# Kernel tuning notes

Measured on AMD Instinct MI355X. Metric: run time of the kernel, lower is better.

The kernel has to match this reference:

```python
import jax, jax.numpy as jnp
import numpy as np

B, NPTS, NBASIS, DIM, H, CH = 8, 1024, 8, 8, 512, 16
EPSILON = 1000.0
P = 2
VOLUME = 2.0 ** DIM  # MC domain [-1,1]^dim


def setup_inputs() -> dict:
    key = jax.random.key(0)
    ks = jax.random.split(key, 10)
    s = jax.random.uniform(ks[0], (NPTS, DIM), dtype=jnp.float32) * 2.0 - 1.0  # MC samples in [-1,1]^dim
    x = jax.random.uniform(ks[1], (1, DIM), dtype=jnp.float32) * 2.0 - 1.0     # eval point
    Wfirst = jax.random.normal(ks[2], (DIM, H), dtype=jnp.float32) / np.sqrt(DIM)
    bfirst = jax.random.normal(ks[3], (H,), dtype=jnp.float32) * 0.01
    Wb = jax.random.normal(ks[4], (NBASIS, H, H), dtype=jnp.float32) / np.sqrt(H)
    bb = jax.random.normal(ks[5], (NBASIS, H), dtype=jnp.float32) * 0.01
    Wlast = jax.random.normal(ks[6], (H, CH), dtype=jnp.float32) / np.sqrt(H)
    blast = jax.random.normal(ks[7], (CH,), dtype=jnp.float32) * 0.01
    Wf = jax.random.normal(ks[8], (DIM, CH), dtype=jnp.float32) / np.sqrt(DIM)
    bf = jax.random.normal(ks[9], (CH,), dtype=jnp.float32) * 0.01
    return dict(s=s, x=x, Wfirst=Wfirst, bfirst=bfirst, Wb=Wb, bb=bb,
                Wlast=Wlast, blast=blast, Wf=Wf, bf=bf)


def _basis_all(pts, Wfirst, bfirst, Wb, bb, Wlast, blast):
    # pts: [M, DIM] -> all n basis nets, batch-repeated: [NBASIS, B, M, CH]
    a0 = jax.nn.elu(jnp.einsum('md,dh->mh', pts, Wfirst) + bfirst)          # [M, H]
    a0 = jnp.broadcast_to(a0[None], (B,) + a0.shape)                         # [B, M, H] (repeat over batch)
    a1 = jax.nn.elu(jnp.einsum('bmh,ihk->ibmk', a0, Wb) + bb[:, None, None, :])  # [n, B, M, H]
    return jnp.einsum('ibmk,kc->ibmc', a1, Wlast) + blast                    # [n, B, M, CH]


def reference(s, x, Wfirst, bfirst, Wb, bb, Wlast, blast, Wf, bf):
    # func(s): linear map realizing the projected function  [NPTS, CH]
    f_s = jnp.einsum('nd,dc->nc', s, Wf) + bf
    basis_s = _basis_all(s, Wfirst, bfirst, Wb, bb, Wlast, blast)            # [n, B, NPTS, CH]
    diff = f_s[None, None] - basis_s                                          # broadcast over n, B
    # Monte Carlo integral of (func - basis_i)^p over [-1,1]^dim, per channel
    integral = VOLUME * jnp.mean(diff ** P, axis=-2)                          # [n, B, CH]
    norm_pc = integral ** (1.0 / P)                                           # Lp norm per channel
    norm_b = jnp.sum(jnp.abs(norm_pc) ** P, axis=-1, keepdims=True) ** (1.0 / P)  # [n, B, 1]
    mu = jnp.where(norm_b <= EPSILON, norm_b, 0.0)                            # [n, B, 1]
    basis_x = _basis_all(x, Wfirst, bfirst, Wb, bb, Wlast, blast)[:, :, 0, :]  # [n, B, CH]
    out = jnp.sum(mu * basis_x, axis=0)                                       # [B, CH]
    normalization = 1e-7 + jnp.sum(mu, axis=0)                                # [B, 1]
    return out / normalization
```

## Files before the change

kernel.cpp:

```cpp
#include <hip/hip_runtime.h>

typedef _Float16 half8 __attribute__((ext_vector_type(8)));
typedef float f32x4 __attribute__((ext_vector_type(4)));
typedef float f32x16 __attribute__((ext_vector_type(16)));
typedef unsigned int u32x4 __attribute__((ext_vector_type(4)));

#define NPTS 1024
#define NB 8
#define HDIM 512
#define CH 16
#define RT 1056

#define OFF_WBF 0u
#define OFF_A0F (4u*1024u*1024u)
#define A0SZ    (64u*RT*16u)
#define OFF_WLF (OFF_A0F + A0SZ)
#define OFF_FS  (OFF_WLF + 16384u)
#define OFF_IS  (OFF_FS + 65536u)
#define OFF_BX  (OFF_IS + 64u)
#define OFF_CT  (OFF_BX + 512u)

__device__ __forceinline__ float elu(float z) { return z > 0.f ? z : expm1f(z); }

__global__ __launch_bounds__(256) void kPrep(const float* __restrict__ s,
    const float* __restrict__ x, const float* __restrict__ Wfirst,
    const float* __restrict__ bfirst, const float* __restrict__ Wb,
    const float* __restrict__ Wlast, const float* __restrict__ Wf,
    const float* __restrict__ bf,
    _Float16* __restrict__ Wbf, _Float16* __restrict__ Wlf,
    _Float16* __restrict__ a0f, float* __restrict__ f_s,
    float* __restrict__ Isum, unsigned* __restrict__ cnt) {
  __shared__ __align__(16) float sm[8192];
  int b = blockIdx.x, t = threadIdx.x;
  if (b < 1024) {
    int i = b >> 7, koct = (b >> 1) & 63, n = (b & 1) * 256 + t;
    const float* src = Wb + ((size_t)i * 512 + koct * 8) * 512 + n;
    float v[8];
#pragma unroll
    for (int j = 0; j < 8; ++j) v[j] = src[j * 512];
    union { _Float16 h[8]; u32x4 u; } hu;
#pragma unroll
    for (int j = 0; j < 8; ++j) hu.h[j] = (_Float16)v[j];
    *(u32x4*)(Wbf + ((size_t)(i * 64 + koct) * 512 + n) * 8) = hu.u;
  } else if (b < 1288) {
    int rr = t >> 6, tl = t & 63;
    int m = (b - 1024) * 4 + rr;
    float* sv = &sm[rr * 8];
    if (tl < 8) sv[tl] = (m < 1024) ? s[m * 8 + tl] : (m == 1024 ? x[tl] : 0.f);
    __syncthreads();
    size_t o = ((size_t)tl * RT + m) * 8;
    if (m <= 1024) {
      float acc[8];
#pragma unroll
      for (int jj = 0; jj < 8; ++jj) acc[jj] = bfirst[8 * tl + jj];
#pragma unroll
      for (int d = 0; d < 8; ++d) {
        float sd = sv[d];
        f32x4 w0 = *(const f32x4*)&Wfirst[d * 512 + 8 * tl];
        f32x4 w1 = *(const f32x4*)&Wfirst[d * 512 + 8 * tl + 4];
#pragma unroll
        for (int e = 0; e < 4; ++e) { acc[e] += sd * w0[e]; acc[4 + e] += sd * w1[e]; }
      }
      union { _Float16 h[8]; u32x4 u; } hu;
#pragma unroll
      for (int jj = 0; jj < 8; ++jj) hu.h[jj] = (_Float16)elu(acc[jj]);
      *(u32x4*)(a0f + o) = hu.u;
      if (m < 1024 && tl < 16) {
        float a = bf[tl];
#pragma unroll
        for (int d = 0; d < 8; ++d) a += sv[d] * Wf[d * 16 + tl];
        f_s[m * 16 + tl] = a;
      }
    } else {
      u32x4 z;
#pragma unroll
      for (int e = 0; e < 4; ++e) z[e] = 0u;
      *(u32x4*)(a0f + o) = z;
    }
  } else {
    if (t < 8) Isum[t] = 0.f;
    if (t == 8) *cnt = 0u;
#pragma unroll
    for (int it = 0; it < 32; ++it) sm[t + 256 * it] = Wlast[t + 256 * it];
    __syncthreads();
#pragma unroll
    for (int p = 0; p < 4; ++p) {
      int oi = p * 256 + t;
      int ko = oi >> 4, ch = oi & 15;
      union { _Float16 h[8]; u32x4 u; } hu;
#pragma unroll
      for (int jj = 0; jj < 8; ++jj) hu.h[jj] = (_Float16)sm[(ko * 8 + jj) * 16 + ch];
      *(u32x4*)(Wlf + oi * 8) = hu.u;
    }
  }
}

__global__ __launch_bounds__(1024, 4) void kB(const _Float16* __restrict__ Wbf,
    const _Float16* __restrict__ a0f, const _Float16* __restrict__ Wlf,
    const float* __restrict__ bb, const float* __restrict__ blast,
    const float* __restrict__ f_s, float* __restrict__ Isum,
    float* __restrict__ basisx, unsigned* __restrict__ cnt,
    float* __restrict__ out) {
  __shared__ u32x4 SC[2048];
  __shared__ float S2[32][16];
  __shared__ float wsum[16];
  __shared__ unsigned oc;
  __shared__ float muL[8];
  int t = threadIdx.x, b = blockIdx.x;
  int i = b & 7, mt = b >> 3;
  int m0 = mt * 32;
  int w = t >> 6, lane = t & 63, ln = lane & 31, q = lane >> 5, q4 = lane >> 4;
  int nw = w * 32;

  const u32x4* a4 = (const u32x4*)a0f;
  const u32x4* b4 = (const u32x4*)Wbf;
  int ma = m0 + ln, nb = nw + ln, ib = i * 64;

  f32x16 acc;
#pragma unroll
  for (int rr = 0; rr < 16; ++rr) acc[rr] = 0.f;

  u32x4 pa[4][2], pb[4][2];
#pragma unroll
  for (int st = 0; st < 3; ++st) {
    int k0 = st * 4 + q, k1 = k0 + 2;
    pa[st][0] = a4[k0 * RT + ma];
    pa[st][1] = a4[k1 * RT + ma];
    pb[st][0] = b4[(size_t)(ib + k0) * 512 + nb];
    pb[st][1] = b4[(size_t)(ib + k1) * 512 + nb];
  }
#pragma unroll
  for (int ks = 0; ks < 16; ++ks) {
    int sl = ks & 3;
    acc = __builtin_amdgcn_mfma_f32_32x32x16_f16(
        __builtin_bit_cast(half8, pa[sl][0]), __builtin_bit_cast(half8, pb[sl][0]), acc, 0, 0, 0);
    acc = __builtin_amdgcn_mfma_f32_32x32x16_f16(
        __builtin_bit_cast(half8, pa[sl][1]), __builtin_bit_cast(half8, pb[sl][1]), acc, 0, 0, 0);
    if (ks < 13) {
      int sn = (ks + 3) & 3;
      int k0 = (ks + 3) * 4 + q, k1 = k0 + 2;
      pa[sn][0] = a4[k0 * RT + ma];
      pa[sn][1] = a4[k1 * RT + ma];
      pb[sn][0] = b4[(size_t)(ib + k0) * 512 + nb];
      pb[sn][1] = b4[(size_t)(ib + k1) * 512 + nb];
    }
  }

  if (t < 512) ((float*)S2)[t] = 0.f;
  __syncthreads();

  float bcol = bb[i * 512 + nw + ln];
  _Float16* scr = (_Float16*)&SC[w * 128];
#pragma unroll
  for (int rr = 0; rr < 16; ++rr) {
    int row = (rr & 3) + 8 * (rr >> 2) + 4 * q;
    float a1 = elu(acc[rr] + bcol);
    int oi = (row >> 4) * 64 + (ln >> 3) * 16 + (row & 15);
    scr[oi * 8 + (ln & 7)] = (_Float16)a1;
  }
  __syncthreads();

  const u32x4* s4 = &SC[w * 128];
  const u32x4* w4 = (const u32x4*)Wlf;
  int ch = lane & 15;
  half8 wv = __builtin_bit_cast(half8, w4[(size_t)((nw >> 3) + q4) * 16 + ch]);
#pragma unroll
  for (int mt2 = 0; mt2 < 2; ++mt2) {
    f32x4 D2;
#pragma unroll
    for (int rr = 0; rr < 4; ++rr) D2[rr] = 0.f;
    half8 pv = __builtin_bit_cast(half8, s4[mt2 * 64 + q4 * 16 + ch]);
    D2 = __builtin_amdgcn_mfma_f32_16x16x32_f16(pv, wv, D2, 0, 0, 0);
#pragma unroll
    for (int rr = 0; rr < 4; ++rr)
      atomicAdd(&S2[mt2 * 16 + q4 * 4 + rr][ch], D2[rr]);
  }
  __syncthreads();

  if (mt == 32) {
    if (t < 16) basisx[i * 16 + t] = S2[0][t] + blast[t];
  } else {
    float loc = 0.f;
    if (t < 512) {
      int ml = t >> 4, c2 = t & 15;
      float bs = S2[ml][c2] + blast[c2];
      float d = f_s[(size_t)(m0 + ml) * 16 + c2] - bs;
      loc = d * d;
    }
    loc += __shfl_xor(loc, 1, 64);
    loc += __shfl_xor(loc, 2, 64);
    loc += __shfl_xor(loc, 4, 64);
    loc += __shfl_xor(loc, 8, 64);
    loc += __shfl_xor(loc, 16, 64);
    loc += __shfl_xor(loc, 32, 64);
    if (lane == 0) wsum[w] = loc;
    __syncthreads();
    if (t == 0) {
      float S = 0.f;
#pragma unroll
      for (int ww = 0; ww < 16; ++ww) S += wsum[ww];
      atomicAdd(&Isum[i], S);
    }
  }

  if (t == 0) {
    __threadfence();
    oc = atomicAdd(cnt, 1u);
  }
  __syncthreads();
  if (oc == 263) {
    __threadfence();
    if (t < 8) {
      float S = atomicAdd(&Isum[t], 0.f);
      float nb = 0.5f * sqrtf(S);
      muL[t] = (nb <= 1000.0f) ? nb : 0.f;
    }
    __syncthreads();
    if (t < 128) {
      int c2 = t & 15;
      float num = 0.f, den = 1e-7f;
#pragma unroll
      for (int ii = 0; ii < NB; ++ii) {
        float bx = atomicAdd(&basisx[ii * 16 + c2], 0.f);
        num += muL[ii] * bx;
        den += muL[ii];
      }
      out[t] = num / den;
    }
  }
}

extern "C" void kernel_launch(void* const* d_in, const int* in_sizes, int n_in,
                              void* d_out, int out_size, void* d_ws, size_t ws_size,
                              hipStream_t stream) {
  const float* s      = (const float*)d_in[0];
  const float* x      = (const float*)d_in[1];
  const float* Wfirst = (const float*)d_in[2];
  const float* bfirst = (const float*)d_in[3];
  const float* Wb     = (const float*)d_in[4];
  const float* bb     = (const float*)d_in[5];
  const float* Wlast  = (const float*)d_in[6];
  const float* blast  = (const float*)d_in[7];
  const float* Wf     = (const float*)d_in[8];
  const float* bf     = (const float*)d_in[9];

  char* ws = (char*)d_ws;
  _Float16* Wbf = (_Float16*)(ws + OFF_WBF);
  _Float16* a0f = (_Float16*)(ws + OFF_A0F);
  _Float16* Wlf = (_Float16*)(ws + OFF_WLF);
  float* f_s    = (float*)(ws + OFF_FS);
  float* Isum   = (float*)(ws + OFF_IS);
  float* basisx = (float*)(ws + OFF_BX);
  unsigned* cnt = (unsigned*)(ws + OFF_CT);
  float* out    = (float*)d_out;

  kPrep<<<1289, 256, 0, stream>>>(s, x, Wfirst, bfirst, Wb, Wlast, Wf, bf,
                                  Wbf, Wlf, a0f, f_s, Isum, cnt);
  kB<<<264, 1024, 0, stream>>>(Wbf, a0f, Wlf, bb, blast, f_s, Isum, basisx, cnt, out);
}
```

Before: 126.6 us.

## Stage GEMM operands through LDS with direct global-to-LDS loads

```diff
diff --git a/kernel.cpp b/kernel.cpp
--- a/kernel.cpp
+++ b/kernel.cpp
@@ -19,6 +19,10 @@
 #define OFF_IS  (OFF_FS + 65536u)
 #define OFF_BX  (OFF_IS + 64u)
 #define OFF_CT  (OFF_BX + 512u)
+
+#define GL2LDS(g, l) __builtin_amdgcn_global_load_lds( \
+    (const __attribute__((address_space(1))) void*)(g), \
+    (__attribute__((address_space(3))) void*)(l), 16, 0, 0)
 
 __device__ __forceinline__ float elu(float z) { return z > 0.f ? z : expm1f(z); }
 
@@ -101,56 +105,60 @@
     const float* __restrict__ f_s, float* __restrict__ Isum,
     float* __restrict__ basisx, unsigned* __restrict__ cnt,
     float* __restrict__ out) {
-  __shared__ u32x4 SC[2048];
-  __shared__ float S2[32][16];
-  __shared__ float wsum[16];
-  __shared__ unsigned oc;
-  __shared__ float muL[8];
+  __shared__ __align__(16) char ALDS[32768];
+  __shared__ __align__(16) char BLDS[32768];
   int t = threadIdx.x, b = blockIdx.x;
   int i = b & 7, mt = b >> 3;
   int m0 = mt * 32;
   int w = t >> 6, lane = t & 63, ln = lane & 31, q = lane >> 5, q4 = lane >> 4;
-  int nw = w * 32;
+  int nw = w * 32, nb = nw + ln, ib = i * 64;
 
   const u32x4* a4 = (const u32x4*)a0f;
   const u32x4* b4 = (const u32x4*)Wbf;
-  int ma = m0 + ln, nb = nw + ln, ib = i * 64;
+  const u32x4* Ald = (const u32x4*)ALDS;
+  const u32x4* Bld = (const u32x4*)BLDS;
+
+#pragma unroll
+  for (int it = 0; it < 2; ++it) {
+    int o = t + 1024 * it;
+    GL2LDS(a4 + ((size_t)(o >> 5) * RT + m0 + (o & 31)), ALDS + o * 16);
+    GL2LDS(b4 + ((size_t)ib * 512 + o), BLDS + o * 16);
+  }
+  __syncthreads();
 
   f32x16 acc;
 #pragma unroll
   for (int rr = 0; rr < 16; ++rr) acc[rr] = 0.f;
 
-  u32x4 pa[4][2], pb[4][2];
-#pragma unroll
-  for (int st = 0; st < 3; ++st) {
-    int k0 = st * 4 + q, k1 = k0 + 2;
-    pa[st][0] = a4[k0 * RT + ma];
-    pa[st][1] = a4[k1 * RT + ma];
-    pb[st][0] = b4[(size_t)(ib + k0) * 512 + nb];
-    pb[st][1] = b4[(size_t)(ib + k1) * 512 + nb];
-  }
-#pragma unroll
-  for (int ks = 0; ks < 16; ++ks) {
-    int sl = ks & 3;
-    acc = __builtin_amdgcn_mfma_f32_32x32x16_f16(
-        __builtin_bit_cast(half8, pa[sl][0]), __builtin_bit_cast(half8, pb[sl][0]), acc, 0, 0, 0);
-    acc = __builtin_amdgcn_mfma_f32_32x32x16_f16(
-        __builtin_bit_cast(half8, pa[sl][1]), __builtin_bit_cast(half8, pb[sl][1]), acc, 0, 0, 0);
-    if (ks < 13) {
-      int sn = (ks + 3) & 3;
-      int k0 = (ks + 3) * 4 + q, k1 = k0 + 2;
-      pa[sn][0] = a4[k0 * RT + ma];
-      pa[sn][1] = a4[k1 * RT + ma];
-      pb[sn][0] = b4[(size_t)(ib + k0) * 512 + nb];
-      pb[sn][1] = b4[(size_t)(ib + k1) * 512 + nb];
-    }
-  }
-
+  for (int c = 0; c < 16; ++c) {
+#pragma unroll
+    for (int s = 0; s < 2; ++s) {
+      int kr = s * 2 + q;
+      half8 aH = __builtin_bit_cast(half8, Ald[(c * 4 + kr) * 32 + ln]);
+      half8 bH = __builtin_bit_cast(half8, Bld[kr * 512 + nb]);
+      acc = __builtin_amdgcn_mfma_f32_32x32x16_f16(aH, bH, acc, 0, 0, 0);
+    }
+    __syncthreads();
+    if (c < 15) {
+#pragma unroll
+      for (int it = 0; it < 2; ++it) {
+        int o = t + 1024 * it;
+        GL2LDS(b4 + ((size_t)(ib + (c + 1) * 4) * 512 + o), BLDS + o * 16);
+      }
+      __syncthreads();
+    }
+  }
+  __syncthreads();
+
+  float (*S2)[16]   = (float(*)[16])ALDS;
+  float* wsum       = (float*)(ALDS + 2048);
+  float* muL        = (float*)(ALDS + 2112);
+  unsigned* ocp     = (unsigned*)(ALDS + 2176);
   if (t < 512) ((float*)S2)[t] = 0.f;
   __syncthreads();
 
   float bcol = bb[i * 512 + nw + ln];
-  _Float16* scr = (_Float16*)&SC[w * 128];
+  _Float16* scr = (_Float16*)(BLDS + w * 2048);
 #pragma unroll
   for (int rr = 0; rr < 16; ++rr) {
     int row = (rr & 3) + 8 * (rr >> 2) + 4 * q;
@@ -160,7 +168,7 @@
   }
   __syncthreads();
 
-  const u32x4* s4 = &SC[w * 128];
+  const u32x4* s4 = (const u32x4*)(BLDS + w * 2048);
   const u32x4* w4 = (const u32x4*)Wlf;
   int ch = lane & 15;
   half8 wv = __builtin_bit_cast(half8, w4[(size_t)((nw >> 3) + q4) * 16 + ch]);
@@ -205,15 +213,15 @@
 
   if (t == 0) {
     __threadfence();
-    oc = atomicAdd(cnt, 1u);
-  }
-  __syncthreads();
-  if (oc == 263) {
+    *ocp = atomicAdd(cnt, 1u);
+  }
+  __syncthreads();
+  if (*ocp == 263) {
     __threadfence();
     if (t < 8) {
       float S = atomicAdd(&Isum[t], 0.f);
-      float nb = 0.5f * sqrtf(S);
-      muL[t] = (nb <= 1000.0f) ? nb : 0.f;
+      float nbv = 0.5f * sqrtf(S);
+      muL[t] = (nbv <= 1000.0f) ? nbv : 0.f;
     }
     __syncthreads();
     if (t < 128) {
```

Measured after the change: 128.4 us. No clear change (+1.4%).

## Fuse first-layer activation into GEMM kernel and split hidden dim across blocks

Applied to the files above, without the earlier changes.

```diff
diff --git a/kernel.cpp b/kernel.cpp
--- a/kernel.cpp
+++ b/kernel.cpp
@@ -9,27 +9,21 @@
 #define NB 8
 #define HDIM 512
 #define CH 16
-#define RT 1056
 
 #define OFF_WBF 0u
-#define OFF_A0F (4u*1024u*1024u)
-#define A0SZ    (64u*RT*16u)
-#define OFF_WLF (OFF_A0F + A0SZ)
-#define OFF_FS  (OFF_WLF + 16384u)
-#define OFF_IS  (OFF_FS + 65536u)
-#define OFF_BX  (OFF_IS + 64u)
-#define OFF_CT  (OFF_BX + 512u)
+#define OFF_WLF 4194304u
+#define OFF_PP  4210688u
+#define OFF_IS  4751360u
+#define OFF_BX  4751424u
+#define OFF_GC  4751936u
 
 __device__ __forceinline__ float elu(float z) { return z > 0.f ? z : expm1f(z); }
 
-__global__ __launch_bounds__(256) void kPrep(const float* __restrict__ s,
-    const float* __restrict__ x, const float* __restrict__ Wfirst,
-    const float* __restrict__ bfirst, const float* __restrict__ Wb,
-    const float* __restrict__ Wlast, const float* __restrict__ Wf,
-    const float* __restrict__ bf,
+__global__ __launch_bounds__(256) void kPrep(const float* __restrict__ Wb,
+    const float* __restrict__ Wlast,
     _Float16* __restrict__ Wbf, _Float16* __restrict__ Wlf,
-    _Float16* __restrict__ a0f, float* __restrict__ f_s,
-    float* __restrict__ Isum, unsigned* __restrict__ cnt) {
+    float* __restrict__ Pp, float* __restrict__ Isum,
+    float* __restrict__ basisx, unsigned* __restrict__ gc) {
   __shared__ __align__(16) float sm[8192];
   int b = blockIdx.x, t = threadIdx.x;
   if (b < 1024) {
@@ -42,44 +36,11 @@
 #pragma unroll
     for (int j = 0; j < 8; ++j) hu.h[j] = (_Float16)v[j];
     *(u32x4*)(Wbf + ((size_t)(i * 64 + koct) * 512 + n) * 8) = hu.u;
-  } else if (b < 1288) {
-    int rr = t >> 6, tl = t & 63;
-    int m = (b - 1024) * 4 + rr;
-    float* sv = &sm[rr * 8];
-    if (tl < 8) sv[tl] = (m < 1024) ? s[m * 8 + tl] : (m == 1024 ? x[tl] : 0.f);
-    __syncthreads();
-    size_t o = ((size_t)tl * RT + m) * 8;
-    if (m <= 1024) {
-      float acc[8];
-#pragma unroll
-      for (int jj = 0; jj < 8; ++jj) acc[jj] = bfirst[8 * tl + jj];
-#pragma unroll
-      for (int d = 0; d < 8; ++d) {
-        float sd = sv[d];
-        f32x4 w0 = *(const f32x4*)&Wfirst[d * 512 + 8 * tl];
-        f32x4 w1 = *(const f32x4*)&Wfirst[d * 512 + 8 * tl + 4];
-#pragma unroll
-        for (int e = 0; e < 4; ++e) { acc[e] += sd * w0[e]; acc[4 + e] += sd * w1[e]; }
-      }
-      union { _Float16 h[8]; u32x4 u; } hu;
-#pragma unroll
-      for (int jj = 0; jj < 8; ++jj) hu.h[jj] = (_Float16)elu(acc[jj]);
-      *(u32x4*)(a0f + o) = hu.u;
-      if (m < 1024 && tl < 16) {
-        float a = bf[tl];
-#pragma unroll
-        for (int d = 0; d < 8; ++d) a += sv[d] * Wf[d * 16 + tl];
-        f_s[m * 16 + tl] = a;
-      }
-    } else {
-      u32x4 z;
-#pragma unroll
-      for (int e = 0; e < 4; ++e) z[e] = 0u;
-      *(u32x4*)(a0f + o) = z;
-    }
-  } else {
+  } else if (b == 1024) {
     if (t < 8) Isum[t] = 0.f;
-    if (t == 8) *cnt = 0u;
+    if (t < 128) basisx[t] = 0.f;
+    gc[t] = 0u;
+    if (t < 9) gc[256 + t] = 0u;
 #pragma unroll
     for (int it = 0; it < 32; ++it) sm[t + 256 * it] = Wlast[t + 256 * it];
     __syncthreads();
@@ -92,65 +53,108 @@
       for (int jj = 0; jj < 8; ++jj) hu.h[jj] = (_Float16)sm[(ko * 8 + jj) * 16 + ch];
       *(u32x4*)(Wlf + oi * 8) = hu.u;
     }
+  } else {
+    int o4 = (b - 1025) * 256 + t;
+    if (o4 < 33792) {
+      f32x4 z; z[0] = 0.f; z[1] = 0.f; z[2] = 0.f; z[3] = 0.f;
+      *(f32x4*)&Pp[o4 * 4] = z;
+    }
   }
 }
 
-__global__ __launch_bounds__(1024, 4) void kB(const _Float16* __restrict__ Wbf,
-    const _Float16* __restrict__ a0f, const _Float16* __restrict__ Wlf,
-    const float* __restrict__ bb, const float* __restrict__ blast,
-    const float* __restrict__ f_s, float* __restrict__ Isum,
-    float* __restrict__ basisx, unsigned* __restrict__ cnt,
-    float* __restrict__ out) {
-  __shared__ u32x4 SC[2048];
-  __shared__ float S2[32][16];
-  __shared__ float wsum[16];
-  __shared__ unsigned oc;
-  __shared__ float muL[8];
+__global__ __launch_bounds__(256, 4) void kB(const _Float16* __restrict__ Wbf,
+    const _Float16* __restrict__ Wlf, const float* __restrict__ s,
+    const float* __restrict__ x, const float* __restrict__ Wfirst,
+    const float* __restrict__ bfirst, const float* __restrict__ Wf,
+    const float* __restrict__ bf, const float* __restrict__ bb,
+    const float* __restrict__ blast, float* __restrict__ Pp,
+    float* __restrict__ Isum, float* __restrict__ basisx,
+    unsigned* __restrict__ gc, float* __restrict__ out) {
+  __shared__ __align__(16) char LB[32768 + 2048 + 256];
+  float* S2f   = (float*)(LB + 32768);
+  float* wsum  = (float*)(LB + 34816);
+  float* muL   = (float*)(LB + 34880);
+  unsigned* ocp  = (unsigned*)(LB + 34944);
+  unsigned* ocgp = (unsigned*)(LB + 34948);
+  const u32x4* Ald = (const u32x4*)LB;
+
   int t = threadIdx.x, b = blockIdx.x;
-  int i = b & 7, mt = b >> 3;
+  int i = b & 7, r = b >> 3;
+  int nq = r & 3, mt = r >> 2;
   int m0 = mt * 32;
   int w = t >> 6, lane = t & 63, ln = lane & 31, q = lane >> 5, q4 = lane >> 4;
-  int nw = w * 32;
-
-  const u32x4* a4 = (const u32x4*)a0f;
+  int nw = nq * 128 + w * 32;
+  int nb = nw + ln, ib = i * 64;
   const u32x4* b4 = (const u32x4*)Wbf;
-  int ma = m0 + ln, nb = nw + ln, ib = i * 64;
-
-  f32x16 acc;
-#pragma unroll
-  for (int rr = 0; rr < 16; ++rr) acc[rr] = 0.f;
-
-  u32x4 pa[4][2], pb[4][2];
+
+  {
+    int m = m0 + (t >> 3), d = t & 7;
+    S2f[t] = (m < 1024) ? s[m * 8 + d] : (m == 1024 ? x[d] : 0.f);
+  }
+
+  u32x4 pb[4][2];
 #pragma unroll
   for (int st = 0; st < 3; ++st) {
     int k0 = st * 4 + q, k1 = k0 + 2;
-    pa[st][0] = a4[k0 * RT + ma];
-    pa[st][1] = a4[k1 * RT + ma];
     pb[st][0] = b4[(size_t)(ib + k0) * 512 + nb];
     pb[st][1] = b4[(size_t)(ib + k1) * 512 + nb];
   }
+  __syncthreads();
+
+  {
+    int ml = t & 31, hq = t >> 5;
+    int hb = hq * 64;
+    float sr[8];
+#pragma unroll
+    for (int d = 0; d < 8; ++d) sr[d] = S2f[ml * 8 + d];
+#pragma unroll
+    for (int oj = 0; oj < 8; ++oj) {
+      int h0 = hb + oj * 8;
+      float a[8];
+      f32x4 b0 = *(const f32x4*)&bfirst[h0];
+      f32x4 b1 = *(const f32x4*)&bfirst[h0 + 4];
+#pragma unroll
+      for (int e = 0; e < 4; ++e) { a[e] = b0[e]; a[4 + e] = b1[e]; }
+#pragma unroll
+      for (int d = 0; d < 8; ++d) {
+        float sd = sr[d];
+        f32x4 w0 = *(const f32x4*)&Wfirst[d * 512 + h0];
+        f32x4 w1 = *(const f32x4*)&Wfirst[d * 512 + h0 + 4];
+#pragma unroll
+        for (int e = 0; e < 4; ++e) { a[e] += sd * w0[e]; a[4 + e] += sd * w1[e]; }
+      }
+      union { _Float16 h[8]; u32x4 u; } hu;
+#pragma unroll
+      for (int e = 0; e < 8; ++e) hu.h[e] = (_Float16)elu(a[e]);
+      ((u32x4*)LB)[(hq * 8 + oj) * 32 + ml] = hu.u;
+    }
+  }
+  __syncthreads();
+
+  f32x16 acc;
+#pragma unroll
+  for (int rr = 0; rr < 16; ++rr) acc[rr] = 0.f;
 #pragma unroll
   for (int ks = 0; ks < 16; ++ks) {
     int sl = ks & 3;
-    acc = __builtin_amdgcn_mfma_f32_32x32x16_f16(
-        __builtin_bit_cast(half8, pa[sl][0]), __builtin_bit_cast(half8, pb[sl][0]), acc, 0, 0, 0);
-    acc = __builtin_amdgcn_mfma_f32_32x32x16_f16(
-        __builtin_bit_cast(half8, pa[sl][1]), __builtin_bit_cast(half8, pb[sl][1]), acc, 0, 0, 0);
+    int k0 = ks * 4 + q, k1 = k0 + 2;
+    half8 aH0 = __builtin_bit_cast(half8, Ald[k0 * 32 + ln]);
+    half8 aH1 = __builtin_bit_cast(half8, Ald[k1 * 32 + ln]);
+    acc = __builtin_amdgcn_mfma_f32_32x32x16_f16(aH0, __builtin_bit_cast(half8, pb[sl][0]), acc, 0, 0, 0);
+    acc = __builtin_amdgcn_mfma_f32_32x32x16_f16(aH1, __builtin_bit_cast(half8, pb[sl][1]), acc, 0, 0, 0);
     if (ks < 13) {
       int sn = (ks + 3) & 3;
-      int k0 = (ks + 3) * 4 + q, k1 = k0 + 2;
-      pa[sn][0] = a4[k0 * RT + ma];
-      pa[sn][1] = a4[k1 * RT + ma];
-      pb[sn][0] = b4[(size_t)(ib + k0) * 512 + nb];
-      pb[sn][1] = b4[(size_t)(ib + k1) * 512 + nb];
-    }
-  }
-
-  if (t < 512) ((float*)S2)[t] = 0.f;
-  __syncthreads();
-
+      int kn0 = (ks + 3) * 4 + q, kn1 = kn0 + 2;
+      pb[sn][0] = b4[(size_t)(ib + kn0) * 512 + nb];
+      pb[sn][1] = b4[(size_t)(ib + kn1) * 512 + nb];
+    }
+  }
+  __syncthreads();
+
+  S2f[t] = 0.f;
+  S2f[t + 256] = 0.f;
   float bcol = bb[i * 512 + nw + ln];
-  _Float16* scr = (_Float16*)&SC[w * 128];
+  _Float16* scr = (_Float16*)(LB + w * 2048);
 #pragma unroll
   for (int rr = 0; rr < 16; ++rr) {
     int row = (rr & 3) + 8 * (rr >> 2) + 4 * q;
@@ -160,10 +164,11 @@
   }
   __syncthreads();
 
-  const u32x4* s4 = &SC[w * 128];
+  const u32x4* s4 = (const u32x4*)(LB + w * 2048);
   const u32x4* w4 = (const u32x4*)Wlf;
   int ch = lane & 15;
   half8 wv = __builtin_bit_cast(half8, w4[(size_t)((nw >> 3) + q4) * 16 + ch]);
+  float (*S2)[16] = (float(*)[16])S2f;
 #pragma unroll
   for (int mt2 = 0; mt2 < 2; ++mt2) {
     f32x4 D2;
@@ -177,55 +182,63 @@
   }
   __syncthreads();
 
-  if (mt == 32) {
-    if (t < 16) basisx[i * 16 + t] = S2[0][t] + blast[t];
-  } else {
-    float loc = 0.f;
-    if (t < 512) {
-      int ml = t >> 4, c2 = t & 15;
-      float bs = S2[ml][c2] + blast[c2];
-      float d = f_s[(size_t)(m0 + ml) * 16 + c2] - bs;
-      loc = d * d;
-    }
-    loc += __shfl_xor(loc, 1, 64);
-    loc += __shfl_xor(loc, 2, 64);
-    loc += __shfl_xor(loc, 4, 64);
-    loc += __shfl_xor(loc, 8, 64);
-    loc += __shfl_xor(loc, 16, 64);
-    loc += __shfl_xor(loc, 32, 64);
-    if (lane == 0) wsum[w] = loc;
+  float* pp = Pp + (size_t)(i * 33 + mt) * 512;
+#pragma unroll
+  for (int p = 0; p < 2; ++p) atomicAdd(&pp[t + 256 * p], S2f[t + 256 * p]);
+  __threadfence();
+  if (t == 0) *ocp = atomicAdd(&gc[mt * 8 + i], 1u);
+  __syncthreads();
+
+  if (*ocp == 3) {
+    __threadfence();
+    if (mt == 32) {
+      if (t < 16) atomicAdd(&basisx[i * 16 + t], atomicAdd(&pp[t], 0.f) + blast[t]);
+    } else {
+      float loc = 0.f;
+#pragma unroll
+      for (int p = 0; p < 2; ++p) {
+        int o = t + 256 * p;
+        int ml = o >> 4, c2 = o & 15;
+        int gm = m0 + ml;
+        float fs = bf[c2];
+#pragma unroll
+        for (int d = 0; d < 8; ++d) fs += s[gm * 8 + d] * Wf[d * 16 + c2];
+        float bs = atomicAdd(&pp[o], 0.f) + blast[c2];
+        float dd = fs - bs;
+        loc += dd * dd;
+      }
+      loc += __shfl_xor(loc, 1, 64);
+      loc += __shfl_xor(loc, 2, 64);
+      loc += __shfl_xor(loc, 4, 64);
+      loc += __shfl_xor(loc, 8, 64);
+      loc += __shfl_xor(loc, 16, 64);
+      loc += __shfl_xor(loc, 32, 64);
+      if (lane == 0) wsum[w] = loc;
+      __syncthreads();
+      if (t == 0) atomicAdd(&Isum[i], wsum[0] + wsum[1] + wsum[2] + wsum[3]);
+    }
+    __threadfence();
+    if (t == 0) *ocgp = atomicAdd(&gc[264], 1u);
     __syncthreads();
-    if (t == 0) {
-      float S = 0.f;
-#pragma unroll
-      for (int ww = 0; ww < 16; ++ww) S += wsum[ww];
-      atomicAdd(&Isum[i], S);
-    }
-  }
-
-  if (t == 0) {
-    __threadfence();
-    oc = atomicAdd(cnt, 1u);
-  }
-  __syncthreads();
-  if (oc == 263) {
-    __threadfence();
-    if (t < 8) {
-      float S = atomicAdd(&Isum[t], 0.f);
-      float nb = 0.5f * sqrtf(S);
-      muL[t] = (nb <= 1000.0f) ? nb : 0.f;
-    }
-    __syncthreads();
-    if (t < 128) {
-      int c2 = t & 15;
-      float num = 0.f, den = 1e-7f;
-#pragma unroll
-      for (int ii = 0; ii < NB; ++ii) {
-        float bx = atomicAdd(&basisx[ii * 16 + c2], 0.f);
-        num += muL[ii] * bx;
-        den += muL[ii];
-      }
-      out[t] = num / den;
+    if (*ocgp == 263) {
+      __threadfence();
+      if (t < 8) {
+        float S = atomicAdd(&Isum[t], 0.f);
+        float nbv = 0.5f * sqrtf(S);
+        muL[t] = (nbv <= 1000.0f) ? nbv : 0.f;
+      }
+      __syncthreads();
+      if (t < 128) {
+        int c2 = t & 15;
+        float num = 0.f, den = 1e-7f;
+#pragma unroll
+        for (int ii = 0; ii < NB; ++ii) {
+          float bx = atomicAdd(&basisx[ii * 16 + c2], 0.f);
+          num += muL[ii] * bx;
+          den += muL[ii];
+        }
+        out[t] = num / den;
+      }
     }
   }
 }
@@ -246,15 +259,14 @@
 
   char* ws = (char*)d_ws;
   _Float16* Wbf = (_Float16*)(ws + OFF_WBF);
-  _Float16* a0f = (_Float16*)(ws + OFF_A0F);
   _Float16* Wlf = (_Float16*)(ws + OFF_WLF);
-  float* f_s    = (float*)(ws + OFF_FS);
+  float* Pp     = (float*)(ws + OFF_PP);
   float* Isum   = (float*)(ws + OFF_IS);
   float* basisx = (float*)(ws + OFF_BX);
-  unsigned* cnt = (unsigned*)(ws + OFF_CT);
+  unsigned* gc  = (unsigned*)(ws + OFF_GC);
   float* out    = (float*)d_out;
 
-  kPrep<<<1289, 256, 0, stream>>>(s, x, Wfirst, bfirst, Wb, Wlast, Wf, bf,
-                                  Wbf, Wlf, a0f, f_s, Isum, cnt);
-  kB<<<264, 1024, 0, stream>>>(Wbf, a0f, Wlf, bb, blast, f_s, Isum, basisx, cnt, out);
+  kPrep<<<1157, 256, 0, stream>>>(Wb, Wlast, Wbf, Wlf, Pp, Isum, basisx, gc);
+  kB<<<1056, 256, 0, stream>>>(Wbf, Wlf, s, x, Wfirst, bfirst, Wf, bf, bb, blast,
+                               Pp, Isum, basisx, gc, out);
 }
```

New measurement: 212.7 us. 1.68x slower.
